# Optimization experiments

Measured on AMD Instinct MI355X. Metric: run time of the kernel, lower is better.

## Reference

```python
import jax, jax.numpy as jnp
import numpy as np

B, C, T = 8, 128, 4096
H = C // 2  # 64


def setup_inputs() -> dict:
    key = jax.random.key(0)
    ks = jax.random.split(key, 9)
    s = 1.0 / np.sqrt(C)
    so = 1.0 / np.sqrt(H)
    return {
        "x": jax.random.normal(ks[0], (B, C, T), dtype=jnp.float32),
        "w_theta": jax.random.normal(ks[1], (H, C), dtype=jnp.float32) * s,
        "b_theta": jax.random.normal(ks[2], (H,), dtype=jnp.float32) * s,
        "w_phi": jax.random.normal(ks[3], (H, C), dtype=jnp.float32) * s,
        "b_phi": jax.random.normal(ks[4], (H,), dtype=jnp.float32) * s,
        "w_g": jax.random.normal(ks[5], (H, C), dtype=jnp.float32) * s,
        "b_g": jax.random.normal(ks[6], (H,), dtype=jnp.float32) * s,
        "w_out": jax.random.normal(ks[7], (C, H), dtype=jnp.float32) * so,
        "b_out": jax.random.normal(ks[8], (C,), dtype=jnp.float32) * so,
    }


def reference(x, w_theta, b_theta, w_phi, b_phi, w_g, b_g, w_out, b_out):
    # 1x1 conv == channel-mixing linear: [B,C,T] -> [B,H,T]
    theta = jnp.einsum("hc,bct->bht", w_theta, x) + b_theta[None, :, None]
    phi = jnp.einsum("hc,bct->bht", w_phi, x) + b_phi[None, :, None]
    g = jnp.einsum("hc,bct->bht", w_g, x) + b_g[None, :, None]
    # scores[b,t,s] = theta[b,:,t] . phi[b,:,s]; softmax over s (last dim)
    scores = jnp.einsum("bht,bhs->bts", theta, phi)  # [B,T,T]
    attn = jax.nn.softmax(scores, axis=-1)
    # out[b,h,t] = sum_s g[b,h,s] * attn[b,t,s]
    out = jnp.einsum("bhs,bts->bht", g, attn)  # [B,H,T]
    out = jnp.einsum("ch,bht->bct", w_out, out) + b_out[None, :, None]
    return x + out
```

## Files before the change

### kernel.cpp

```cpp
#include <hip/hip_runtime.h>
#include <hip/hip_bf16.h>

typedef _Float16 half_t;
typedef half_t halfx8 __attribute__((ext_vector_type(8)));
typedef half_t halfx4 __attribute__((ext_vector_type(4)));
typedef half_t halfx2 __attribute__((ext_vector_type(2)));
typedef __fp16 fp16x2 __attribute__((ext_vector_type(2)));
typedef float f32x4 __attribute__((ext_vector_type(4)));
typedef float f32x16 __attribute__((ext_vector_type(16)));
typedef int i32x4 __attribute__((ext_vector_type(4)));

#define B_ 8
#define C_ 128
#define T_ 4096
#define H_ 64
#define L2E 1.44269504088896340736f

static __device__ __forceinline__ halfx2 pk2(float a, float b) {
    fp16x2 r = __builtin_amdgcn_cvt_pkrtz(a, b);
    return __builtin_bit_cast(halfx2, r);
}
static __device__ __forceinline__ int pk2i(float a, float b) {
    return __builtin_bit_cast(int, __builtin_amdgcn_cvt_pkrtz(a, b));
}
static __device__ __forceinline__ int swz(int row, int col) {
    return (row << 6) + (col ^ ((row & 7) << 3));
}

__global__ __launch_bounds__(256) void proj_kernel(
    const float* __restrict__ x,
    const float* __restrict__ w_theta, const float* __restrict__ b_theta,
    const float* __restrict__ w_phi,   const float* __restrict__ b_phi,
    const float* __restrict__ w_g,     const float* __restrict__ b_g,
    half_t* __restrict__ Q, half_t* __restrict__ Ko, half_t* __restrict__ Vt)
{
    __shared__ __align__(16) half_t xt[64][136];
    __shared__ __align__(16) half_t ts[64][72];

    const int tid  = threadIdx.x;
    const int lane = tid & 63;
    const int wave = tid >> 6;
    const int b    = blockIdx.x >> 6;
    const int t0   = (blockIdx.x & 63) << 6;

    const int rowA  = lane & 15;
    const int kgrp  = lane >> 4;
    const int row_d = kgrp << 2;

    const float* xb = x + (size_t)b * C_ * T_ + t0;
    #pragma unroll
    for (int it = 0; it < 8; ++it) {
        int li = it * 256 + tid;
        int c  = li >> 4;
        int tc = li & 15;
        f32x4 v = *(const f32x4*)(xb + (size_t)c * T_ + tc * 4);
        #pragma unroll
        for (int j = 0; j < 4; ++j) xt[tc * 4 + j][c] = (half_t)v[j];
    }

    const int h0 = wave << 4;
    const float* Ws[3] = {w_theta, w_phi, w_g};
    const float* Bs[3] = {b_theta, b_phi, b_g};
    halfx8 wa[3][4];
    #pragma unroll
    for (int m = 0; m < 3; ++m) {
        const float* wrow = Ws[m] + (size_t)(h0 + rowA) * C_;
        #pragma unroll
        for (int cc = 0; cc < 4; ++cc) {
            const float* p = wrow + cc * 32 + kgrp * 8;
            f32x4 a = *(const f32x4*)p;
            f32x4 c2 = *(const f32x4*)(p + 4);
            halfx8 f;
            f[0]=(half_t)a[0]; f[1]=(half_t)a[1]; f[2]=(half_t)a[2]; f[3]=(half_t)a[3];
            f[4]=(half_t)c2[0];f[5]=(half_t)c2[1];f[6]=(half_t)c2[2];f[7]=(half_t)c2[3];
            wa[m][cc] = f;
        }
    }

    __syncthreads();

    #pragma unroll
    for (int m = 0; m < 3; ++m) {
        f32x4 acc[4] = {};
        #pragma unroll
        for (int tt = 0; tt < 4; ++tt) {
            #pragma unroll
            for (int cc = 0; cc < 4; ++cc) {
                halfx8 bfrag = *(const halfx8*)&xt[tt * 16 + rowA][cc * 32 + kgrp * 8];
                acc[tt] = __builtin_amdgcn_mfma_f32_16x16x32_f16(wa[m][cc], bfrag, acc[tt], 0, 0, 0);
            }
        }
        float bias[4];
        #pragma unroll
        for (int r = 0; r < 4; ++r) bias[r] = Bs[m][h0 + row_d + r];

        if (m < 2) {
            const float sc = (m == 0) ? L2E : 1.0f;
            #pragma unroll
            for (int tt = 0; tt < 4; ++tt)
                #pragma unroll
                for (int r = 0; r < 4; ++r)
                    ts[tt * 16 + rowA][h0 + row_d + r] = (half_t)((acc[tt][r] + bias[r]) * sc);
            __syncthreads();
            half_t* dst = (m == 0 ? Q : Ko) + ((size_t)b * T_ + t0) * H_;
            #pragma unroll
            for (int it = 0; it < 2; ++it) {
                int q = it * 256 + tid;
                int t = q >> 3, hc = q & 7;
                *(halfx8*)(dst + (size_t)t * H_ + hc * 8) = *(const halfx8*)&ts[t][hc * 8];
            }
            __syncthreads();
        } else {
            half_t* dst = Vt + (size_t)b * H_ * T_ + t0;
            #pragma unroll
            for (int tt = 0; tt < 4; ++tt)
                #pragma unroll
                for (int r = 0; r < 4; ++r)
                    dst[(size_t)(h0 + row_d + r) * T_ + tt * 16 + rowA] = (half_t)(acc[tt][r] + bias[r]);
        }
    }
}

__global__ __launch_bounds__(256, 4) void attn_kernel(
    const half_t* __restrict__ Q, const half_t* __restrict__ K,
    const half_t* __restrict__ Vt, half_t* __restrict__ Op,
    float* __restrict__ Mp, float* __restrict__ Lp, int NS)
{
    __shared__ __align__(16) half_t Ks[2][64 * 64];
    __shared__ __align__(16) half_t Vs[2][64 * 64];

    const int tid  = threadIdx.x;
    const int wave = tid >> 6;
    const int lane = tid & 63;
    const int qb   = blockIdx.x / NS;
    const int sp   = blockIdx.x - qb * NS;
    const int b    = qb >> 5;
    const int t0   = (qb & 31) << 7;
    const int q0   = t0 + wave * 32;
    const int lq   = lane & 31;
    const int hi   = lane >> 5;
    const int NT   = T_ / (64 * NS);
    const int sbase = sp * (T_ / NS);

    halfx8 qf[4];
    const half_t* qr = Q + ((size_t)b * T_ + q0 + lq) * H_ + hi * 8;
    #pragma unroll
    for (int kc = 0; kc < 4; ++kc) qf[kc] = *(const halfx8*)(qr + kc * 16);

    f32x16 oacc[2] = {};
    float mr = -INFINITY, lr = 0.f;

    const int r0 = tid >> 3;
    const int c8 = (tid & 7) * 8;
    const half_t* kp = K  + (size_t)b * T_ * H_ + (size_t)(sbase + r0) * H_ + c8;
    const half_t* vp = Vt + (size_t)b * H_ * T_ + (size_t)r0 * T_ + sbase + c8;

    halfx8 rK0 = *(const halfx8*)kp;
    halfx8 rK1 = *(const halfx8*)(kp + 32 * H_);
    halfx8 rV0 = *(const halfx8*)vp;
    halfx8 rV1 = *(const halfx8*)(vp + 32 * T_);
    kp += 64 * H_; vp += 64;

    *(halfx8*)&Ks[0][swz(r0, c8)]      = rK0;
    *(halfx8*)&Ks[0][swz(r0 + 32, c8)] = rK1;
    *(halfx8*)&Vs[0][swz(r0, c8)]      = rV0;
    *(halfx8*)&Vs[0][swz(r0 + 32, c8)] = rV1;
    __syncthreads();

    for (int t = 0; t < NT; ++t) {
        const int cur = t & 1;
        const bool more = (t + 1 < NT);
        if (more) {
            rK0 = *(const halfx8*)kp;
            rK1 = *(const halfx8*)(kp + 32 * H_);
            rV0 = *(const halfx8*)vp;
            rV1 = *(const halfx8*)(vp + 32 * T_);
            kp += 64 * H_; vp += 64;
        }

        f32x16 sacc[2] = {};
        __builtin_amdgcn_s_setprio(1);
        #pragma unroll
        for (int st = 0; st < 2; ++st)
            #pragma unroll
            for (int kc = 0; kc < 4; ++kc) {
                halfx8 kf = *(const halfx8*)&Ks[cur][swz(st * 32 + lq, kc * 16 + hi * 8)];
                sacc[st] = __builtin_amdgcn_mfma_f32_32x32x16_f16(kf, qf[kc], sacc[st], 0, 0, 0);
            }
        __builtin_amdgcn_s_setprio(0);

        float pm = sacc[0][0];
        #pragma unroll
        for (int st = 0; st < 2; ++st)
            #pragma unroll
            for (int r = 0; r < 16; ++r)
                pm = fmaxf(pm, sacc[st][r]);
        pm = fmaxf(pm, __shfl_xor(pm, 32));
        if (__any(pm > mr + 8.f)) {
            float mnew  = fmaxf(mr, pm);
            float scale = exp2f(mr - mnew);
            mr = mnew; lr *= scale;
            #pragma unroll
            for (int dt = 0; dt < 2; ++dt)
                #pragma unroll
                for (int r = 0; r < 16; ++r) oacc[dt][r] *= scale;
        }
        float ps = 0.f;
        #pragma unroll
        for (int st = 0; st < 2; ++st)
            #pragma unroll
            for (int r = 0; r < 16; ++r) {
                float p = exp2f(sacc[st][r] - mr);
                sacc[st][r] = p;
                ps += p;
            }
        lr += ps + __shfl_xor(ps, 32);

        halfx8 pfrag[4];
        #pragma unroll
        for (int sc = 0; sc < 4; ++sc) {
            const int st = sc >> 1, rb = (sc & 1) * 8;
            int d0 = pk2i(sacc[st][rb + 0], sacc[st][rb + 1]);
            int d1 = pk2i(sacc[st][rb + 2], sacc[st][rb + 3]);
            int e0 = pk2i(sacc[st][rb + 4], sacc[st][rb + 5]);
            int e1 = pk2i(sacc[st][rb + 6], sacc[st][rb + 7]);
            int s0 = hi ? d0 : e0;
            int s1 = hi ? d1 : e1;
            int g0 = __shfl_xor(s0, 32);
            int g1 = __shfl_xor(s1, 32);
            i32x4 w;
            w[0] = hi ? g0 : d0;
            w[1] = hi ? g1 : d1;
            w[2] = hi ? e0 : g0;
            w[3] = hi ? e1 : g1;
            pfrag[sc] = __builtin_bit_cast(halfx8, w);
        }

        __builtin_amdgcn_s_setprio(1);
        #pragma unroll
        for (int dt = 0; dt < 2; ++dt)
            #pragma unroll
            for (int sc = 0; sc < 4; ++sc) {
                halfx8 vf = *(const halfx8*)&Vs[cur][swz(dt * 32 + lq, sc * 16 + hi * 8)];
                oacc[dt] = __builtin_amdgcn_mfma_f32_32x32x16_f16(vf, pfrag[sc], oacc[dt], 0, 0, 0);
            }
        __builtin_amdgcn_s_setprio(0);

        if (more) {
            const int nxt = cur ^ 1;
            *(halfx8*)&Ks[nxt][swz(r0, c8)]      = rK0;
            *(halfx8*)&Ks[nxt][swz(r0 + 32, c8)] = rK1;
            *(halfx8*)&Vs[nxt][swz(r0, c8)]      = rV0;
            *(halfx8*)&Vs[nxt][swz(r0 + 32, c8)] = rV1;
            __syncthreads();
        }
    }

    const int BT = B_ * T_;
    const int grow = b * T_ + q0 + lq;
    float inv = 1.f / lr;
    half_t* od = Op + ((size_t)sp * BT + grow) * H_;
    #pragma unroll
    for (int dt = 0; dt < 2; ++dt)
        #pragma unroll
        for (int g = 0; g < 4; ++g) {
            union { halfx2 h2[2]; halfx4 h4; } u;
            u.h2[0] = pk2(oacc[dt][g * 4 + 0] * inv, oacc[dt][g * 4 + 1] * inv);
            u.h2[1] = pk2(oacc[dt][g * 4 + 2] * inv, oacc[dt][g * 4 + 3] * inv);
            *(halfx4*)(od + dt * 32 + g * 8 + hi * 4) = u.h4;
        }
    if (Mp != nullptr && hi == 0) {
        Mp[(size_t)sp * BT + grow] = mr;
        Lp[(size_t)sp * BT + grow] = lr;
    }
}

__global__ __launch_bounds__(256) void merge_kernel(
    const half_t* __restrict__ Op, const float* __restrict__ Mp,
    const float* __restrict__ Lp, half_t* __restrict__ O, int NS)
{
    const int idx = blockIdx.x * 256 + threadIdx.x;
    const int row = idx >> 3;
    const int hc  = (idx & 7) * 8;
    const int BT  = B_ * T_;

    float m = -INFINITY;
    for (int s = 0; s < NS; ++s) m = fmaxf(m, Mp[(size_t)s * BT + row]);
    float W = 0.f;
    float acc[8] = {};
    for (int s = 0; s < NS; ++s) {
        float w = Lp[(size_t)s * BT + row] * exp2f(Mp[(size_t)s * BT + row] - m);
        W += w;
        halfx8 o = *(const halfx8*)(Op + ((size_t)s * BT + row) * H_ + hc);
        #pragma unroll
        for (int j = 0; j < 8; ++j) acc[j] += w * (float)o[j];
    }
    float inv = 1.f / W;
    halfx8 r;
    #pragma unroll
    for (int j = 0; j < 8; ++j) r[j] = (half_t)(acc[j] * inv);
    *(halfx8*)(O + (size_t)row * H_ + hc) = r;
}

__global__ __launch_bounds__(256) void outproj_kernel(
    const half_t* __restrict__ O, const float* __restrict__ w_out,
    const float* __restrict__ b_out, const float* __restrict__ x,
    float* __restrict__ out)
{
    __shared__ __align__(16) half_t Ot[64][72];

    const int tid  = threadIdx.x;
    const int lane = tid & 63;
    const int wave = tid >> 6;
    const int b    = blockIdx.x >> 6;
    const int t0   = (blockIdx.x & 63) << 6;

    const int rowA  = lane & 15;
    const int kgrp  = lane >> 4;
    const int row_d = kgrp << 2;

    #pragma unroll
    for (int it = 0; it < 2; ++it) {
        int q = it * 256 + tid;
        int t = q >> 3, hc = q & 7;
        *(halfx8*)&Ot[t][hc * 8] = *(const halfx8*)(O + ((size_t)b * T_ + t0 + t) * H_ + hc * 8);
    }

    const int c0 = wave * 32;
    halfx8 wf[2][2];
    #pragma unroll
    for (int ct = 0; ct < 2; ++ct) {
        const float* wrow = w_out + (size_t)(c0 + ct * 16 + rowA) * H_;
        #pragma unroll
        for (int hc = 0; hc < 2; ++hc) {
            const float* p = wrow + hc * 32 + kgrp * 8;
            f32x4 a = *(const f32x4*)p;
            f32x4 c2 = *(const f32x4*)(p + 4);
            halfx8 f;
            f[0]=(half_t)a[0]; f[1]=(half_t)a[1]; f[2]=(half_t)a[2]; f[3]=(half_t)a[3];
            f[4]=(half_t)c2[0];f[5]=(half_t)c2[1];f[6]=(half_t)c2[2];f[7]=(half_t)c2[3];
            wf[ct][hc] = f;
        }
    }

    __syncthreads();

    #pragma unroll
    for (int ct = 0; ct < 2; ++ct) {
        #pragma unroll
        for (int tt = 0; tt < 4; ++tt) {
            f32x4 acc = {};
            #pragma unroll
            for (int hc = 0; hc < 2; ++hc) {
                halfx8 of = *(const halfx8*)&Ot[tt * 16 + rowA][hc * 32 + kgrp * 8];
                acc = __builtin_amdgcn_mfma_f32_16x16x32_f16(wf[ct][hc], of, acc, 0, 0, 0);
            }
            const int c = c0 + ct * 16 + row_d;
            const size_t base = (size_t)b * C_ * T_ + t0 + tt * 16 + rowA;
            #pragma unroll
            for (int r = 0; r < 4; ++r) {
                size_t idx = base + (size_t)(c + r) * T_;
                out[idx] = x[idx] + b_out[c + r] + acc[r];
            }
        }
    }
}

extern "C" void kernel_launch(void* const* d_in, const int* in_sizes, int n_in,
                              void* d_out, int out_size, void* d_ws, size_t ws_size,
                              hipStream_t stream) {
    const float* x       = (const float*)d_in[0];
    const float* w_theta = (const float*)d_in[1];
    const float* b_theta = (const float*)d_in[2];
    const float* w_phi   = (const float*)d_in[3];
    const float* b_phi   = (const float*)d_in[4];
    const float* w_g     = (const float*)d_in[5];
    const float* b_g     = (const float*)d_in[6];
    const float* w_out   = (const float*)d_in[7];
    const float* b_out   = (const float*)d_in[8];
    float* out = (float*)d_out;

    const size_t mat = (size_t)B_ * T_ * H_;
    const size_t BT  = (size_t)B_ * T_;
    half_t* Qw = (half_t*)d_ws;
    half_t* Kw = Qw + mat;
    half_t* Vw = Kw + mat;
    half_t* Ow = Vw + mat;
    const size_t base_b = 4 * mat * sizeof(half_t);

    auto need = [&](size_t ns) { return base_b + ns * mat * 2 + ns * BT * 8; };
    const int NS = (ws_size >= need(4)) ? 4 : ((ws_size >= need(2)) ? 2 : 1);

    half_t* Opart = Ow;
    float*  Mp = nullptr;
    float*  Lp = nullptr;
    if (NS > 1) {
        Opart = (half_t*)((char*)d_ws + base_b);
        Mp = (float*)((char*)d_ws + base_b + (size_t)NS * mat * 2);
        Lp = Mp + (size_t)NS * BT;
    }

    proj_kernel<<<dim3(B_ * (T_ / 64)), dim3(256), 0, stream>>>(
        x, w_theta, b_theta, w_phi, b_phi, w_g, b_g, Qw, Kw, Vw);
    attn_kernel<<<dim3(B_ * (T_ / 128) * NS), dim3(256), 0, stream>>>(
        Qw, Kw, Vw, Opart, Mp, Lp, NS);
    if (NS > 1)
        merge_kernel<<<dim3((int)(BT * H_ / (256 * 8))), dim3(256), 0, stream>>>(
            Opart, Mp, Lp, Ow, NS);
    outproj_kernel<<<dim3(B_ * (T_ / 64)), dim3(256), 0, stream>>>(Ow, w_out, b_out, x, out);
}
```

Before: 89.61 us.

## Permute V shared layout to drop P shuffles; compute row sums via MFMA

V tiles are written to shared memory in a permuted half4 layout, so the P fragments can be fed to the PV MFMA directly from the softmax accumulator registers, removing the cross-half lane shuffles and selects. The softmax denominator is now accumulated with an extra MFMA against a ones vector instead of a scalar sum plus shuffle. The max reduction uses a 3-input max tree and defers the cross-half shuffle into the rescale branch. In exchange there is one extra MFMA per 16-wide chunk and narrower shared stores for V.

```diff
diff --git a/kernel.cpp b/kernel.cpp
--- a/kernel.cpp
+++ b/kernel.cpp
@@ -23,8 +23,14 @@
 static __device__ __forceinline__ int pk2i(float a, float b) {
     return __builtin_bit_cast(int, __builtin_amdgcn_cvt_pkrtz(a, b));
 }
+static __device__ __forceinline__ float max3f(float a, float b, float c) {
+    return fmaxf(fmaxf(a, b), c);
+}
 static __device__ __forceinline__ int swz(int row, int col) {
     return (row << 6) + (col ^ ((row & 7) << 3));
+}
+static __device__ __forceinline__ int swz4(int row, int col) {
+    return (row << 6) + ((col & ~7) ^ ((row & 7) << 3)) + (col & 7);
 }
 
 __global__ __launch_bounds__(256) void proj_kernel(
@@ -147,11 +153,17 @@
     #pragma unroll
     for (int kc = 0; kc < 4; ++kc) qf[kc] = *(const halfx8*)(qr + kc * 16);
 
+    halfx8 ones;
+    #pragma unroll
+    for (int j = 0; j < 8; ++j) ones[j] = (half_t)1.0f;
+
     f32x16 oacc[2] = {};
-    float mr = -INFINITY, lr = 0.f;
+    f32x16 lacc = {};
+    float mr = -INFINITY;
 
     const int r0 = tid >> 3;
     const int c8 = (tid & 7) * 8;
+    const int gA = (c8 & ~15) + ((c8 & 8) >> 1);
     const half_t* kp = K  + (size_t)b * T_ * H_ + (size_t)(sbase + r0) * H_ + c8;
     const half_t* vp = Vt + (size_t)b * H_ * T_ + (size_t)r0 * T_ + sbase + c8;
 
@@ -161,10 +173,16 @@
     halfx8 rV1 = *(const halfx8*)(vp + 32 * T_);
     kp += 64 * H_; vp += 64;
 
-    *(halfx8*)&Ks[0][swz(r0, c8)]      = rK0;
-    *(halfx8*)&Ks[0][swz(r0 + 32, c8)] = rK1;
-    *(halfx8*)&Vs[0][swz(r0, c8)]      = rV0;
-    *(halfx8*)&Vs[0][swz(r0 + 32, c8)] = rV1;
+    {
+        *(halfx8*)&Ks[0][swz(r0, c8)]      = rK0;
+        *(halfx8*)&Ks[0][swz(r0 + 32, c8)] = rK1;
+        union { halfx8 h8; halfx4 h4[2]; } u0, u1;
+        u0.h8 = rV0; u1.h8 = rV1;
+        *(halfx4*)&Vs[0][swz4(r0, gA)]          = u0.h4[0];
+        *(halfx4*)&Vs[0][swz4(r0, gA + 8)]      = u0.h4[1];
+        *(halfx4*)&Vs[0][swz4(r0 + 32, gA)]     = u1.h4[0];
+        *(halfx4*)&Vs[0][swz4(r0 + 32, gA + 8)] = u1.h4[1];
+    }
     __syncthreads();
 
     for (int t = 0; t < NT; ++t) {
@@ -189,75 +207,81 @@
             }
         __builtin_amdgcn_s_setprio(0);
 
-        float pm = sacc[0][0];
-        #pragma unroll
-        for (int st = 0; st < 2; ++st)
-            #pragma unroll
-            for (int r = 0; r < 16; ++r)
-                pm = fmaxf(pm, sacc[st][r]);
-        pm = fmaxf(pm, __shfl_xor(pm, 32));
+        float pm;
+        {
+            float a0 = max3f(sacc[0][0],  sacc[0][1],  sacc[0][2]);
+            float a1 = max3f(sacc[0][3],  sacc[0][4],  sacc[0][5]);
+            float a2 = max3f(sacc[0][6],  sacc[0][7],  sacc[0][8]);
+            float a3 = max3f(sacc[0][9],  sacc[0][10], sacc[0][11]);
+            float a4 = max3f(sacc[0][12], sacc[0][13], sacc[0][14]);
+            float b0 = max3f(sacc[1][0],  sacc[1][1],  sacc[1][2]);
+            float b1 = max3f(sacc[1][3],  sacc[1][4],  sacc[1][5]);
+            float b2 = max3f(sacc[1][6],  sacc[1][7],  sacc[1][8]);
+            float b3 = max3f(sacc[1][9],  sacc[1][10], sacc[1][11]);
+            float b4 = max3f(sacc[1][12], sacc[1][13], sacc[1][14]);
+            float c0 = max3f(a0, a1, a2);
+            float c1 = max3f(a3, a4, sacc[0][15]);
+            float c2 = max3f(b0, b1, b2);
+            float c3 = max3f(b3, b4, sacc[1][15]);
+            pm = max3f(max3f(c0, c1, c2), c3, -INFINITY);
+        }
         if (__any(pm > mr + 8.f)) {
+            pm = fmaxf(pm, __shfl_xor(pm, 32));
             float mnew  = fmaxf(mr, pm);
             float scale = exp2f(mr - mnew);
-            mr = mnew; lr *= scale;
+            mr = mnew;
+            lacc[0] *= scale;
             #pragma unroll
             for (int dt = 0; dt < 2; ++dt)
                 #pragma unroll
                 for (int r = 0; r < 16; ++r) oacc[dt][r] *= scale;
         }
-        float ps = 0.f;
         #pragma unroll
         for (int st = 0; st < 2; ++st)
             #pragma unroll
-            for (int r = 0; r < 16; ++r) {
-                float p = exp2f(sacc[st][r] - mr);
-                sacc[st][r] = p;
-                ps += p;
-            }
-        lr += ps + __shfl_xor(ps, 32);
+            for (int r = 0; r < 16; ++r)
+                sacc[st][r] = exp2f(sacc[st][r] - mr);
 
         halfx8 pfrag[4];
         #pragma unroll
         for (int sc = 0; sc < 4; ++sc) {
             const int st = sc >> 1, rb = (sc & 1) * 8;
-            int d0 = pk2i(sacc[st][rb + 0], sacc[st][rb + 1]);
-            int d1 = pk2i(sacc[st][rb + 2], sacc[st][rb + 3]);
-            int e0 = pk2i(sacc[st][rb + 4], sacc[st][rb + 5]);
-            int e1 = pk2i(sacc[st][rb + 6], sacc[st][rb + 7]);
-            int s0 = hi ? d0 : e0;
-            int s1 = hi ? d1 : e1;
-            int g0 = __shfl_xor(s0, 32);
-            int g1 = __shfl_xor(s1, 32);
             i32x4 w;
-            w[0] = hi ? g0 : d0;
-            w[1] = hi ? g1 : d1;
-            w[2] = hi ? e0 : g0;
-            w[3] = hi ? e1 : g1;
+            w[0] = pk2i(sacc[st][rb + 0], sacc[st][rb + 1]);
+            w[1] = pk2i(sacc[st][rb + 2], sacc[st][rb + 3]);
+            w[2] = pk2i(sacc[st][rb + 4], sacc[st][rb + 5]);
+            w[3] = pk2i(sacc[st][rb + 6], sacc[st][rb + 7]);
             pfrag[sc] = __builtin_bit_cast(halfx8, w);
         }
 
         __builtin_amdgcn_s_setprio(1);
         #pragma unroll
-        for (int dt = 0; dt < 2; ++dt)
-            #pragma unroll
-            for (int sc = 0; sc < 4; ++sc) {
-                halfx8 vf = *(const halfx8*)&Vs[cur][swz(dt * 32 + lq, sc * 16 + hi * 8)];
-                oacc[dt] = __builtin_amdgcn_mfma_f32_32x32x16_f16(vf, pfrag[sc], oacc[dt], 0, 0, 0);
-            }
+        for (int sc = 0; sc < 4; ++sc) {
+            halfx8 vf0 = *(const halfx8*)&Vs[cur][swz(lq,      sc * 16 + hi * 8)];
+            halfx8 vf1 = *(const halfx8*)&Vs[cur][swz(32 + lq, sc * 16 + hi * 8)];
+            oacc[0] = __builtin_amdgcn_mfma_f32_32x32x16_f16(vf0, pfrag[sc], oacc[0], 0, 0, 0);
+            oacc[1] = __builtin_amdgcn_mfma_f32_32x32x16_f16(vf1, pfrag[sc], oacc[1], 0, 0, 0);
+            lacc    = __builtin_amdgcn_mfma_f32_32x32x16_f16(ones, pfrag[sc], lacc, 0, 0, 0);
+        }
         __builtin_amdgcn_s_setprio(0);
 
         if (more) {
             const int nxt = cur ^ 1;
             *(halfx8*)&Ks[nxt][swz(r0, c8)]      = rK0;
             *(halfx8*)&Ks[nxt][swz(r0 + 32, c8)] = rK1;
-            *(halfx8*)&Vs[nxt][swz(r0, c8)]      = rV0;
-            *(halfx8*)&Vs[nxt][swz(r0 + 32, c8)] = rV1;
+            union { halfx8 h8; halfx4 h4[2]; } u0, u1;
+            u0.h8 = rV0; u1.h8 = rV1;
+            *(halfx4*)&Vs[nxt][swz4(r0, gA)]          = u0.h4[0];
+            *(halfx4*)&Vs[nxt][swz4(r0, gA + 8)]      = u0.h4[1];
+            *(halfx4*)&Vs[nxt][swz4(r0 + 32, gA)]     = u1.h4[0];
+            *(halfx4*)&Vs[nxt][swz4(r0 + 32, gA + 8)] = u1.h4[1];
             __syncthreads();
         }
     }
 
     const int BT = B_ * T_;
     const int grow = b * T_ + q0 + lq;
+    const float lr = lacc[0];
     float inv = 1.f / lr;
     half_t* od = Op + ((size_t)sp * BT + grow) * H_;
     #pragma unroll
```

Result: slower. 107.6 us (+20.0%).
